# Performance work log

Hardware: AMD Instinct MI355X
Metric: run time of the kernel (lower is better)

The kernel has to match this reference:

```python
import jax, jax.numpy as jnp
import numpy as np

D_MODEL = 1024
D_INNER = 2 * D_MODEL          # expand=2
D_STATE = 16
D_CONV = 4
DT_RANK = D_MODEL // 16        # ceil(1024/16)
BATCH, SEQ = 4, 1024
LN_EPS = 1e-5
LRELU_SLOPE = 0.01


def setup_inputs() -> dict:
    key = jax.random.key(0)
    ks = jax.random.split(key, 12)
    s = 0.02
    return {
        "x": jax.random.normal(ks[0], (BATCH, SEQ, D_MODEL), jnp.float32),
        "W_in": jax.random.normal(ks[1], (D_MODEL, 2 * D_INNER), jnp.float32) * s,
        "conv_w": jax.random.normal(ks[2], (D_INNER, D_CONV), jnp.float32) * s,
        "conv_b": jnp.zeros((D_INNER,), jnp.float32),
        "W_x": jax.random.normal(ks[3], (D_INNER, DT_RANK + 2 * D_STATE), jnp.float32) * s,
        "W_dt": jax.random.normal(ks[4], (DT_RANK, D_INNER), jnp.float32) * s,
        "b_dt": jax.random.normal(ks[5], (D_INNER,), jnp.float32) * 0.1 - 4.0,
        "A_log": jnp.log(jnp.broadcast_to(jnp.arange(1, D_STATE + 1, dtype=jnp.float32), (D_INNER, D_STATE))),
        "D": jnp.ones((D_INNER,), jnp.float32),
        "W_out": jax.random.normal(ks[6], (D_INNER, D_MODEL), jnp.float32) * s,
        "gamma": jnp.ones((D_MODEL,), jnp.float32),
        "beta": jnp.zeros((D_MODEL,), jnp.float32),
    }


def _selective_scan(u, dt, A, B, C, Dp):
    # u, dt: (b, l, d); A: (d, n); B, C: (b, l, n); Dp: (d,)
    dA = jnp.exp(dt[..., None] * A)                       # (b, l, d, n)
    dBu = dt[..., None] * B[:, :, None, :] * u[..., None]  # (b, l, d, n)

    def step(h, inp):
        dA_t, dBu_t, C_t = inp                            # (b,d,n),(b,d,n),(b,n)
        h = dA_t * h + dBu_t
        y = jnp.einsum("bdn,bn->bd", h, C_t)
        return h, y

    h0 = jnp.zeros((u.shape[0], u.shape[2], A.shape[1]), u.dtype)
    xs = (dA.transpose(1, 0, 2, 3), dBu.transpose(1, 0, 2, 3), C.transpose(1, 0, 2))
    _, ys = jax.lax.scan(step, h0, xs)                    # ys: (l, b, d)
    return ys.transpose(1, 0, 2) + u * Dp                 # (b, l, d)


def _mamba(x, W_in, conv_w, conv_b, W_x, W_dt, b_dt, A_log, Dp, W_out):
    xz = x @ W_in                                          # (b, l, 2*di)
    xc, z = jnp.split(xz, 2, axis=-1)
    # causal depthwise conv over time
    xc_t = xc.transpose(0, 2, 1)                           # (b, di, l)
    kern = conv_w[:, None, :]                              # (di, 1, k)
    conv = jax.lax.conv_general_dilated(
        xc_t, kern, window_strides=(1,), padding=[(D_CONV - 1, 0)],
        dimension_numbers=("NCH", "OIH", "NCH"), feature_group_count=D_INNER)
    xc = jax.nn.silu(conv + conv_b[None, :, None]).transpose(0, 2, 1)  # (b, l, di)

    x_dbl = xc @ W_x                                       # (b, l, dt_rank + 2n)
    dt, Bm, Cm = jnp.split(x_dbl, [DT_RANK, DT_RANK + D_STATE], axis=-1)
    dt = jax.nn.softplus(dt @ W_dt + b_dt)                 # (b, l, di)
    A = -jnp.exp(A_log)                                    # (di, n)

    y = _selective_scan(xc, dt, A, Bm, Cm, Dp)             # (b, l, di)
    y = y * jax.nn.silu(z)
    return y @ W_out                                       # (b, l, d_model)


def reference(x, W_in, conv_w, conv_b, W_x, W_dt, b_dt, A_log, D, W_out, gamma, beta):
    h = x + _mamba(x, W_in, conv_w, conv_b, W_x, W_dt, b_dt, A_log, D, W_out)
    mu = jnp.mean(h, axis=-1, keepdims=True)
    var = jnp.mean(jnp.square(h - mu), axis=-1, keepdims=True)
    h = (h - mu) * jax.lax.rsqrt(var + LN_EPS) * gamma + beta
    return jnp.where(h >= 0, h, LRELU_SLOPE * h)
```

## Files before the change

kernel.cpp:

```cpp
#include <hip/hip_runtime.h>
#include <hip/hip_fp16.h>
#include <cstdint>
#include <cstddef>

typedef _Float16 f16x8 __attribute__((ext_vector_type(8)));
typedef _Float16 f16x4 __attribute__((ext_vector_type(4)));
typedef float    f32x4 __attribute__((ext_vector_type(4)));

#define TC  64
#define NCH 16

__device__ __forceinline__ float sigmoidf_(float x) { return 1.f / (1.f + __expf(-x)); }

__device__ __forceinline__ void gload_lds16(const _Float16* g, _Float16* l) {
  __builtin_amdgcn_global_load_lds(
      (const __attribute__((address_space(1))) void*)g,
      (__attribute__((address_space(3))) void*)l, 16, 0, 0);
}

__device__ __forceinline__ void t16_body(const float* __restrict__ src,
    _Float16* __restrict__ dst, int R, int C, int Cpad, int bx, int by,
    int tid, float tile[32][33]) {
  int c0 = bx * 32, r0 = by * 32, tx = tid & 31, ty = tid >> 5;
  #pragma unroll
  for (int i = 0; i < 4; ++i) {
    int r = r0 + ty + i * 8, c = c0 + tx;
    tile[ty + i * 8][tx] = (r < R && c < C) ? src[(size_t)r * C + c] : 0.f;
  }
  __syncthreads();
  #pragma unroll
  for (int i = 0; i < 4; ++i) {
    int cc = c0 + ty + i * 8, rr = r0 + tx;
    if (cc < Cpad && rr < R) dst[(size_t)cc * R + rr] = (_Float16)tile[tx][ty + i * 8];
  }
}

__global__ __launch_bounds__(256) void k_prep(
    const float* __restrict__ x, _Float16* __restrict__ x16,
    const float* __restrict__ W_in, _Float16* __restrict__ WinT,
    const float* __restrict__ W_x, _Float16* __restrict__ WxT,
    const float* __restrict__ W_dt, _Float16* __restrict__ WdtT,
    const float* __restrict__ W_out, _Float16* __restrict__ WoutT,
    const float* __restrict__ convw, _Float16* __restrict__ cwT)
{
  __shared__ float tile[32][33];
  const int blk = blockIdx.x, tid = threadIdx.x;
  if (blk < 4096) {
    int i = blk * 256 + tid;
    float4 v = ((const float4*)x)[i];
    f16x4 o = {(_Float16)v.x, (_Float16)v.y, (_Float16)v.z, (_Float16)v.w};
    ((f16x4*)x16)[i] = o;
  } else if (blk < 8192) {
    int b = blk - 4096;
    t16_body(W_in, WinT, 1024, 4096, 4096, b & 127, b >> 7, tid, tile);
  } else if (blk < 8448) {
    int b = blk - 8192;
    t16_body(W_x, WxT, 2048, 96, 128, b & 3, b >> 2, tid, tile);
  } else if (blk < 8576) {
    int b = blk - 8448;
    t16_body(W_dt, WdtT, 64, 2048, 2048, b & 63, b >> 6, tid, tile);
  } else if (blk < 10624) {
    int b = blk - 8576;
    t16_body(W_out, WoutT, 2048, 1024, 1024, b & 31, b >> 5, tid, tile);
  } else {
    #pragma unroll
    for (int j = 0; j < 32; ++j) {
      int idx = j * 256 + tid;
      int tap = idx >> 11, d = idx & 2047;
      cwT[idx] = (_Float16)convw[d * 4 + tap];
    }
  }
}

template <int EPI>
__global__ __launch_bounds__(256) void k_gemm_bt(
    const _Float16* __restrict__ A,
    const _Float16* __restrict__ BT,
    float* __restrict__ C,
    _Float16* __restrict__ C16,
    _Float16* __restrict__ AUX,
    const float* __restrict__ bias,
    int M, int N, int K)
{
  __shared__ __align__(16) _Float16 As[128 * 64];
  __shared__ __align__(16) _Float16 Bs[128 * 64];
  const int tid  = threadIdx.x;
  const int lane = tid & 63;
  const int wave = tid >> 6;
  const int wm = (wave >> 1) * 64;
  const int wn = (wave & 1) * 64;
  const int l15 = lane & 15;
  const int q   = lane >> 4;
  const int m0 = blockIdx.y * 128;
  const int n0 = blockIdx.x * 128;

  const int kpb = K / gridDim.z;
  const int k0  = blockIdx.z * kpb;

  const int rch = lane >> 3;
  const int g   = (lane & 7) ^ (rch & 7);
  const _Float16* gA = A  + (size_t)(m0 + wave * 32 + rch) * K + k0 + g * 8;
  const _Float16* gB = BT + (size_t)(n0 + wave * 32 + rch) * K + k0 + g * 8;
  _Float16* lA = As + wave * 32 * 64 + lane * 8;
  _Float16* lB = Bs + wave * 32 * 64 + lane * 8;

  const int sx = l15 & 7;

  f32x4 acc[4][4] = {};

  for (int k = 0; k < kpb; k += 64) {
    #pragma unroll
    for (int c = 0; c < 4; ++c) {
      gload_lds16(gA + (size_t)(c * 8) * K + k, lA + c * 512);
      gload_lds16(gB + (size_t)(c * 8) * K + k, lB + c * 512);
    }
    __syncthreads();
    #pragma unroll
    for (int k32 = 0; k32 < 2; ++k32) {
      f16x8 af[4], bf[4];
      #pragma unroll
      for (int i = 0; i < 4; ++i) {
        af[i] = *(const f16x8*)&As[(wm + i * 16 + l15) * 64 + ((k32 * 4 + q) ^ sx) * 8];
        bf[i] = *(const f16x8*)&Bs[(wn + i * 16 + l15) * 64 + ((k32 * 4 + q) ^ sx) * 8];
      }
      #pragma unroll
      for (int mi = 0; mi < 4; ++mi)
        #pragma unroll
        for (int ni = 0; ni < 4; ++ni)
          acc[mi][ni] = __builtin_amdgcn_mfma_f32_16x16x32_f16(af[mi], bf[ni], acc[mi][ni], 0, 0, 0);
    }
    __syncthreads();
  }

  if constexpr (EPI == 4) {
    #pragma unroll
    for (int mi = 0; mi < 4; ++mi) {
      #pragma unroll
      for (int ni = 0; ni < 4; ++ni) {
        int col = n0 + wn + ni * 16 + l15;
        #pragma unroll
        for (int r = 0; r < 4; ++r) {
          int row = m0 + wm + mi * 16 + q * 4 + r;
          C[(size_t)blockIdx.z * M * N + (size_t)row * N + col] = acc[mi][ni][r];
        }
      }
    }
  } else {
    _Float16* Ep = As + wave * 1280;
    const int rr = lane >> 2, cb = lane & 3;
    #pragma unroll
    for (int mi = 0; mi < 4; ++mi) {
      #pragma unroll
      for (int ni = 0; ni < 4; ++ni) {
        int col = n0 + wn + ni * 16 + l15;
        #pragma unroll
        for (int r = 0; r < 4; ++r) {
          float v = acc[mi][ni][r];
          _Float16 hv;
          if constexpr (EPI == 2) {
            float t = v + bias[col];
            float sp = (t > 20.f) ? t : log1pf(__expf(t));
            hv = (_Float16)sp;
          } else if constexpr (EPI == 3) {
            hv = (n0 >= 2048) ? (_Float16)(v * sigmoidf_(v)) : (_Float16)v;
          } else {
            hv = (_Float16)v;
          }
          Ep[(q * 4 + r) * 72 + ni * 16 + l15] = hv;
        }
      }
      __syncthreads();
      f16x8 o0 = *(const f16x8*)&Ep[rr * 72 + cb * 16];
      f16x8 o1 = *(const f16x8*)&Ep[rr * 72 + cb * 16 + 8];
      int row = m0 + wm + mi * 16 + rr;
      int colb = wn + cb * 16;
      if constexpr (EPI == 2) {
        _Float16* dst = AUX + (size_t)row * N + n0 + colb;
        *(f16x8*)dst = o0;
        *(f16x8*)(dst + 8) = o1;
      } else if constexpr (EPI == 3) {
        if (n0 < 2048) {
          _Float16* dst = C16 + (size_t)row * 2048 + n0 + colb;
          *(f16x8*)dst = o0;
          *(f16x8*)(dst + 8) = o1;
        } else {
          _Float16* dst = AUX + (size_t)row * 2048 + (n0 - 2048) + colb;
          *(f16x8*)dst = o0;
          *(f16x8*)(dst + 8) = o1;
        }
      } else {
        _Float16* dst = C16 + (size_t)blockIdx.z * M * N + (size_t)row * N + n0 + colb;
        *(f16x8*)dst = o0;
        *(f16x8*)(dst + 8) = o1;
      }
      __syncthreads();
    }
  }
}

__global__ __launch_bounds__(256) void k_red(const float* __restrict__ Cp,
                                             _Float16* __restrict__ dtin,
                                             float* __restrict__ xbc) {
  int i = blockIdx.x * 256 + threadIdx.x;
  const int PL = 4096 * 128;
  float s = Cp[i] + Cp[i + PL] + Cp[i + 2 * PL] + Cp[i + 3 * PL];
  int col = i & 127, row = i >> 7;
  if (col < 64) dtin[(size_t)row * 64 + col] = (_Float16)s;
  else if (col < 96) xbc[(size_t)row * 32 + (col - 64)] = s;
}

__global__ __launch_bounds__(256) void k_conv_silu(
    const _Float16* __restrict__ xc, const _Float16* __restrict__ cwT,
    const float* __restrict__ cb, _Float16* __restrict__ out)
{
  const int row = blockIdx.x;
  const int t = row & 1023;
  const int d8 = threadIdx.x;
  const size_t base = (size_t)row * 2048 + d8 * 8;
  f16x8 p0 = *(const f16x8*)&xc[base];
  f16x8 w3 = *(const f16x8*)&cwT[3 * 2048 + d8 * 8];
  float4 cb0 = ((const float4*)cb)[d8 * 2];
  float4 cb1 = ((const float4*)cb)[d8 * 2 + 1];
  float accv[8] = {cb0.x, cb0.y, cb0.z, cb0.w, cb1.x, cb1.y, cb1.z, cb1.w};
  #pragma unroll
  for (int j = 0; j < 8; ++j) accv[j] += (float)w3[j] * (float)p0[j];
  if (t >= 1) {
    f16x8 p = *(const f16x8*)&xc[base - 2048];
    f16x8 w = *(const f16x8*)&cwT[2 * 2048 + d8 * 8];
    #pragma unroll
    for (int j = 0; j < 8; ++j) accv[j] += (float)w[j] * (float)p[j];
  }
  if (t >= 2) {
    f16x8 p = *(const f16x8*)&xc[base - 4096];
    f16x8 w = *(const f16x8*)&cwT[1 * 2048 + d8 * 8];
    #pragma unroll
    for (int j = 0; j < 8; ++j) accv[j] += (float)w[j] * (float)p[j];
  }
  if (t >= 3) {
    f16x8 p = *(const f16x8*)&xc[base - 6144];
    f16x8 w = *(const f16x8*)&cwT[0 * 2048 + d8 * 8];
    #pragma unroll
    for (int j = 0; j < 8; ++j) accv[j] += (float)w[j] * (float)p[j];
  }
  f16x8 o;
  #pragma unroll
  for (int j = 0; j < 8; ++j) o[j] = (_Float16)(accv[j] * sigmoidf_(accv[j]));
  *(f16x8*)&out[base] = o;
}

__global__ __launch_bounds__(256) void k_scan_part(
    const _Float16* __restrict__ dt, const _Float16* __restrict__ u,
    const float* __restrict__ xbc, const float* __restrict__ A_log,
    float* __restrict__ P, float* __restrict__ S)
{
  const int tid = threadIdx.x;
  const int d = blockIdx.x * 256 + tid;
  const int c = blockIdx.y;
  const int b = blockIdx.z;
  const int row0 = b * 1024 + c * TC;
  __shared__ float Bs[TC * 16];
  for (int i = tid; i < TC * 16; i += 256) {
    int t = i >> 4, n = i & 15;
    Bs[i] = xbc[(size_t)(row0 + t) * 32 + n];
  }
  float a[16];
  #pragma unroll
  for (int n = 0; n < 16; ++n) a[n] = -__expf(A_log[d * 16 + n]);
  float h[16] = {};
  float sumdt = 0.f;
  __syncthreads();
  for (int t = 0; t < TC; ++t) {
    const int row = row0 + t;
    float dtv = (float)dt[(size_t)row * 2048 + d];
    float uv  = (float)u[(size_t)row * 2048 + d];
    float dtu = dtv * uv;
    sumdt += dtv;
    #pragma unroll
    for (int n = 0; n < 16; ++n)
      h[n] = h[n] * __expf(dtv * a[n]) + dtu * Bs[t * 16 + n];
  }
  const size_t base = (size_t)(b * NCH + c) * 16 * 2048 + d;
  #pragma unroll
  for (int n = 0; n < 16; ++n) {
    P[base + n * 2048] = __expf(sumdt * a[n]);
    S[base + n * 2048] = h[n];
  }
}

__global__ __launch_bounds__(256) void k_scan_comb(
    float* __restrict__ P, const float* __restrict__ S)
{
  int idx = blockIdx.x * 256 + threadIdx.x;
  int d = idx & 2047;
  int n = (idx >> 11) & 15;
  int b = idx >> 15;
  float H = 0.f;
  for (int c = 0; c < NCH - 1; ++c) {
    size_t off = ((size_t)(b * NCH + c) * 16 + n) * 2048 + d;
    H = P[off] * H + S[off];
    P[off] = H;
  }
}

__global__ __launch_bounds__(256) void k_scan_y(
    const _Float16* dt, const _Float16* __restrict__ u,
    const _Float16* __restrict__ zs, const float* __restrict__ xbc,
    const float* __restrict__ A_log, const float* __restrict__ Hbuf,
    const float* __restrict__ Dv, _Float16* ys)
{
  const int tid = threadIdx.x;
  const int d = blockIdx.x * 256 + tid;
  const int c = blockIdx.y;
  const int b = blockIdx.z;
  const int row0 = b * 1024 + c * TC;
  __shared__ float Bs[TC * 16], Cs[TC * 16];
  for (int i = tid; i < TC * 16; i += 256) {
    int t = i >> 4, n = i & 15;
    Bs[i] = xbc[(size_t)(row0 + t) * 32 + n];
    Cs[i] = xbc[(size_t)(row0 + t) * 32 + 16 + n];
  }
  float a[16];
  #pragma unroll
  for (int n = 0; n < 16; ++n) a[n] = -__expf(A_log[d * 16 + n]);
  float h[16];
  if (c == 0) {
    #pragma unroll
    for (int n = 0; n < 16; ++n) h[n] = 0.f;
  } else {
    const size_t hb = (size_t)(b * NCH + (c - 1)) * 16 * 2048 + d;
    #pragma unroll
    for (int n = 0; n < 16; ++n) h[n] = Hbuf[hb + n * 2048];
  }
  const float Dd = Dv[d];
  __syncthreads();
  for (int t = 0; t < TC; ++t) {
    const int row = row0 + t;
    float dtv = (float)dt[(size_t)row * 2048 + d];
    float uv  = (float)u[(size_t)row * 2048 + d];
    float zv  = (float)zs[(size_t)row * 2048 + d];
    float dtu = dtv * uv;
    float y = uv * Dd;
    #pragma unroll
    for (int n = 0; n < 16; ++n) {
      h[n] = h[n] * __expf(dtv * a[n]) + dtu * Bs[t * 16 + n];
      y = fmaf(h[n], Cs[t * 16 + n], y);
    }
    ys[(size_t)row * 2048 + d] = (_Float16)(y * zv);
  }
}

__global__ __launch_bounds__(256) void k_resid_ln(
    const float* __restrict__ x, const _Float16* __restrict__ yp,
    const float* __restrict__ gamma, const float* __restrict__ beta,
    float* __restrict__ out)
{
  int row = blockIdx.x;
  int tid = threadIdx.x;
  const int PLH = 4096 * 1024;
  const int o4 = row * 256 + tid;
  float4 xv = ((const float4*)x)[o4];
  f16x4 a0 = ((const f16x4*)yp)[o4];
  f16x4 a1 = ((const f16x4*)(yp + PLH))[o4];
  float v[4] = {xv.x + (float)a0[0] + (float)a1[0],
                xv.y + (float)a0[1] + (float)a1[1],
                xv.z + (float)a0[2] + (float)a1[2],
                xv.w + (float)a0[3] + (float)a1[3]};
  float s = v[0] + v[1] + v[2] + v[3];
  float s2 = v[0]*v[0] + v[1]*v[1] + v[2]*v[2] + v[3]*v[3];
  #pragma unroll
  for (int off = 32; off > 0; off >>= 1) {
    s  += __shfl_down(s, off, 64);
    s2 += __shfl_down(s2, off, 64);
  }
  __shared__ float rs[4], rs2[4];
  int wv = tid >> 6, ln = tid & 63;
  if (ln == 0) { rs[wv] = s; rs2[wv] = s2; }
  __syncthreads();
  if (tid == 0) {
    float a = 0.f, b2 = 0.f;
    #pragma unroll
    for (int i = 0; i < 4; ++i) { a += rs[i]; b2 += rs2[i]; }
    rs[0] = a; rs2[0] = b2;
  }
  __syncthreads();
  float mu  = rs[0] * (1.f / 1024.f);
  float var = rs2[0] * (1.f / 1024.f) - mu * mu;
  float inv = rsqrtf(var + 1e-5f);
  float4 gv = ((const float4*)gamma)[tid];
  float4 bv = ((const float4*)beta)[tid];
  float gg[4] = {gv.x, gv.y, gv.z, gv.w};
  float bb[4] = {bv.x, bv.y, bv.z, bv.w};
  float4 ov;
  float* op = (float*)&ov;
  #pragma unroll
  for (int i = 0; i < 4; ++i) {
    float hn = (v[i] - mu) * inv * gg[i] + bb[i];
    op[i] = hn >= 0.f ? hn : 0.01f * hn;
  }
  ((float4*)out)[o4] = ov;
}

extern "C" void kernel_launch(void* const* d_in, const int* in_sizes, int n_in,
                              void* d_out, int out_size, void* d_ws, size_t ws_size,
                              hipStream_t stream)
{
  const float* x     = (const float*)d_in[0];
  const float* W_in  = (const float*)d_in[1];
  const float* convw = (const float*)d_in[2];
  const float* convb = (const float*)d_in[3];
  const float* W_x   = (const float*)d_in[4];
  const float* W_dt  = (const float*)d_in[5];
  const float* b_dt  = (const float*)d_in[6];
  const float* A_log = (const float*)d_in[7];
  const float* Dv    = (const float*)d_in[8];
  const float* W_out = (const float*)d_in[9];
  const float* gamma = (const float*)d_in[10];
  const float* beta  = (const float*)d_in[11];
  float* out = (float*)d_out;

  char* ws = (char*)d_ws;
  const size_t MB = 1ull << 20;
  _Float16* x16   = (_Float16*)(ws + 0 * MB);
  _Float16* WinT  = (_Float16*)(ws + 8 * MB);
  _Float16* xc16  = (_Float16*)(ws + 16 * MB);
  _Float16* zsil  = (_Float16*)(ws + 32 * MB);
  _Float16* xcs   = (_Float16*)(ws + 48 * MB);
  _Float16* dtb   = (_Float16*)(ws + 64 * MB);
  _Float16* WxT   = (_Float16*)(ws + 80 * MB);
  _Float16* WdtT  = (_Float16*)(ws + 80 * MB + 512 * 1024);
  _Float16* WoutT = (_Float16*)(ws + 81 * MB);
  float*    Cpart = (float*)   (ws + 85 * MB);
  float*    xbc   = (float*)   (ws + 93 * MB);
  _Float16* dtin  = (_Float16*)(ws + 93 * MB + 512 * 1024);
  _Float16* cwT   = (_Float16*)(ws + 94 * MB);
  float*    Pb    = (float*)   (ws + 0 * MB);
  float*    Sb    = (float*)   (ws + 8 * MB);
  _Float16* ysb   = dtb;
  _Float16* ypH   = (_Float16*)(ws + 0 * MB);

  k_prep<<<10625, 256, 0, stream>>>(x, x16, W_in, WinT, W_x, WxT, W_dt, WdtT,
                                    W_out, WoutT, convw, cwT);
  k_gemm_bt<3><<<dim3(32, 32), 256, 0, stream>>>(x16, WinT, nullptr, xc16, zsil, nullptr, 4096, 4096, 1024);
  k_conv_silu<<<4096, 256, 0, stream>>>(xc16, cwT, convb, xcs);
  k_gemm_bt<4><<<dim3(1, 32, 4), 256, 0, stream>>>(xcs, WxT, Cpart, nullptr, nullptr, nullptr, 4096, 128, 2048);
  k_red<<<4096 * 128 / 256, 256, 0, stream>>>(Cpart, dtin, xbc);
  k_gemm_bt<2><<<dim3(16, 32), 256, 0, stream>>>(dtin, WdtT, nullptr, nullptr, dtb, b_dt, 4096, 2048, 64);
  k_scan_part<<<dim3(8, NCH, 4), 256, 0, stream>>>(dtb, xcs, xbc, A_log, Pb, Sb);
  k_scan_comb<<<4 * 16 * 2048 / 256, 256, 0, stream>>>(Pb, Sb);
  k_scan_y<<<dim3(8, NCH, 4), 256, 0, stream>>>(dtb, xcs, zsil, xbc, A_log, Pb, Dv, ysb);
  k_gemm_bt<5><<<dim3(8, 32, 2), 256, 0, stream>>>(ysb, WoutT, nullptr, ypH, nullptr, nullptr, 4096, 1024, 2048);
  k_resid_ln<<<4096, 256, 0, stream>>>(x, ypH, gamma, beta, out);
}
```

Baseline: 364.7 us.

## Fuse causal conv+SiLU into x_proj GEMM and scan kernels, drop conv kernel

Removes the standalone conv+SiLU kernel and its 16 MB fp16 output buffer. The conv and SiLU are now recomputed inside the x-projection GEMM's A-tile load and inside both scan kernels, using a rolling window of the previous three timesteps. The residual LayerNorm now reads the fp16 copy of x instead of fp32, and workspace buffers are remapped. This trades extra global reads and recomputation for fewer memory passes and one fewer launch, and the fp16 residual slightly lowers precision.

```diff
diff --git a/kernel.cpp b/kernel.cpp
--- a/kernel.cpp
+++ b/kernel.cpp
@@ -76,7 +76,6 @@
 __global__ __launch_bounds__(256) void k_gemm_bt(
     const _Float16* __restrict__ A,
     const _Float16* __restrict__ BT,
-    float* __restrict__ C,
     _Float16* __restrict__ C16,
     _Float16* __restrict__ AUX,
     const float* __restrict__ bias,
@@ -132,68 +131,147 @@
     __syncthreads();
   }
 
-  if constexpr (EPI == 4) {
-    #pragma unroll
-    for (int mi = 0; mi < 4; ++mi) {
-      #pragma unroll
-      for (int ni = 0; ni < 4; ++ni) {
-        int col = n0 + wn + ni * 16 + l15;
-        #pragma unroll
-        for (int r = 0; r < 4; ++r) {
-          int row = m0 + wm + mi * 16 + q * 4 + r;
-          C[(size_t)blockIdx.z * M * N + (size_t)row * N + col] = acc[mi][ni][r];
+  _Float16* Ep = As + wave * 1280;
+  const int rr = lane >> 2, cb2 = lane & 3;
+  #pragma unroll
+  for (int mi = 0; mi < 4; ++mi) {
+    #pragma unroll
+    for (int ni = 0; ni < 4; ++ni) {
+      int col = n0 + wn + ni * 16 + l15;
+      #pragma unroll
+      for (int r = 0; r < 4; ++r) {
+        float v = acc[mi][ni][r];
+        _Float16 hv;
+        if constexpr (EPI == 2) {
+          float t = v + bias[col];
+          float sp = (t > 20.f) ? t : log1pf(__expf(t));
+          hv = (_Float16)sp;
+        } else if constexpr (EPI == 3) {
+          hv = (n0 >= 2048) ? (_Float16)(v * sigmoidf_(v)) : (_Float16)v;
+        } else {
+          hv = (_Float16)v;
         }
+        Ep[(q * 4 + r) * 72 + ni * 16 + l15] = hv;
       }
     }
-  } else {
-    _Float16* Ep = As + wave * 1280;
-    const int rr = lane >> 2, cb = lane & 3;
-    #pragma unroll
-    for (int mi = 0; mi < 4; ++mi) {
-      #pragma unroll
-      for (int ni = 0; ni < 4; ++ni) {
-        int col = n0 + wn + ni * 16 + l15;
-        #pragma unroll
-        for (int r = 0; r < 4; ++r) {
-          float v = acc[mi][ni][r];
-          _Float16 hv;
-          if constexpr (EPI == 2) {
-            float t = v + bias[col];
-            float sp = (t > 20.f) ? t : log1pf(__expf(t));
-            hv = (_Float16)sp;
-          } else if constexpr (EPI == 3) {
-            hv = (n0 >= 2048) ? (_Float16)(v * sigmoidf_(v)) : (_Float16)v;
-          } else {
-            hv = (_Float16)v;
-          }
-          Ep[(q * 4 + r) * 72 + ni * 16 + l15] = hv;
-        }
-      }
-      __syncthreads();
-      f16x8 o0 = *(const f16x8*)&Ep[rr * 72 + cb * 16];
-      f16x8 o1 = *(const f16x8*)&Ep[rr * 72 + cb * 16 + 8];
-      int row = m0 + wm + mi * 16 + rr;
-      int colb = wn + cb * 16;
-      if constexpr (EPI == 2) {
-        _Float16* dst = AUX + (size_t)row * N + n0 + colb;
+    __syncthreads();
+    f16x8 o0 = *(const f16x8*)&Ep[rr * 72 + cb2 * 16];
+    f16x8 o1 = *(const f16x8*)&Ep[rr * 72 + cb2 * 16 + 8];
+    int row = m0 + wm + mi * 16 + rr;
+    int colb = wn + cb2 * 16;
+    if constexpr (EPI == 2) {
+      _Float16* dst = AUX + (size_t)row * N + n0 + colb;
+      *(f16x8*)dst = o0;
+      *(f16x8*)(dst + 8) = o1;
+    } else if constexpr (EPI == 3) {
+      if (n0 < 2048) {
+        _Float16* dst = C16 + (size_t)row * 2048 + n0 + colb;
         *(f16x8*)dst = o0;
         *(f16x8*)(dst + 8) = o1;
-      } else if constexpr (EPI == 3) {
-        if (n0 < 2048) {
-          _Float16* dst = C16 + (size_t)row * 2048 + n0 + colb;
-          *(f16x8*)dst = o0;
-          *(f16x8*)(dst + 8) = o1;
-        } else {
-          _Float16* dst = AUX + (size_t)row * 2048 + (n0 - 2048) + colb;
-          *(f16x8*)dst = o0;
-          *(f16x8*)(dst + 8) = o1;
-        }
       } else {
-        _Float16* dst = C16 + (size_t)blockIdx.z * M * N + (size_t)row * N + n0 + colb;
+        _Float16* dst = AUX + (size_t)row * 2048 + (n0 - 2048) + colb;
         *(f16x8*)dst = o0;
         *(f16x8*)(dst + 8) = o1;
       }
-      __syncthreads();
+    } else {
+      _Float16* dst = C16 + (size_t)blockIdx.z * M * N + (size_t)row * N + n0 + colb;
+      *(f16x8*)dst = o0;
+      *(f16x8*)(dst + 8) = o1;
+    }
+    __syncthreads();
+  }
+}
+
+__global__ __launch_bounds__(256) void k_g2(
+    const _Float16* __restrict__ xc,
+    const _Float16* __restrict__ cwT,
+    const float* __restrict__ cb,
+    const _Float16* __restrict__ BT,
+    float* __restrict__ C)
+{
+  __shared__ __align__(16) _Float16 As[128 * 64];
+  __shared__ __align__(16) _Float16 Bs[128 * 64];
+  const int tid  = threadIdx.x;
+  const int lane = tid & 63;
+  const int wave = tid >> 6;
+  const int wm = (wave >> 1) * 64;
+  const int wn = (wave & 1) * 64;
+  const int l15 = lane & 15;
+  const int q   = lane >> 4;
+  const int m0 = blockIdx.y * 128;
+  const int K = 2048;
+  const int k0 = blockIdx.z * 512;
+
+  const int rch = lane >> 3;
+  const int g   = (lane & 7) ^ (rch & 7);
+  const _Float16* gB = BT + (size_t)(wave * 32 + rch) * K + k0 + g * 8;
+  _Float16* lB = Bs + wave * 32 * 64 + lane * 8;
+  _Float16* lA = As + wave * 2048 + lane * 8;
+
+  const int sx = l15 & 7;
+
+  f32x4 acc[4][4] = {};
+
+  for (int k = 0; k < 512; k += 64) {
+    #pragma unroll
+    for (int c = 0; c < 4; ++c)
+      gload_lds16(gB + (size_t)(c * 8) * K + k, lB + c * 512);
+    #pragma unroll
+    for (int c = 0; c < 4; ++c) {
+      int row = wave * 32 + c * 8 + rch;
+      int m = m0 + row;
+      int t = m & 1023;
+      int dcol = k0 + k + g * 8;
+      const _Float16* xp = xc + (size_t)m * 2048 + dcol;
+      f16x8 x0 = *(const f16x8*)xp;
+      f16x8 x1 = {}, x2 = {}, x3 = {};
+      if (t >= 1) x1 = *(const f16x8*)(xp - 2048);
+      if (t >= 2) x2 = *(const f16x8*)(xp - 4096);
+      if (t >= 3) x3 = *(const f16x8*)(xp - 6144);
+      f16x8 w3 = *(const f16x8*)&cwT[3 * 2048 + dcol];
+      f16x8 w2 = *(const f16x8*)&cwT[2 * 2048 + dcol];
+      f16x8 w1 = *(const f16x8*)&cwT[1 * 2048 + dcol];
+      f16x8 w0 = *(const f16x8*)&cwT[0 * 2048 + dcol];
+      float4 cb0 = *(const float4*)&cb[dcol];
+      float4 cb1 = *(const float4*)&cb[dcol + 4];
+      float av[8] = {cb0.x, cb0.y, cb0.z, cb0.w, cb1.x, cb1.y, cb1.z, cb1.w};
+      f16x8 o;
+      #pragma unroll
+      for (int j = 0; j < 8; ++j) {
+        float s = av[j] + (float)w3[j] * (float)x0[j] + (float)w2[j] * (float)x1[j]
+                        + (float)w1[j] * (float)x2[j] + (float)w0[j] * (float)x3[j];
+        o[j] = (_Float16)(s * sigmoidf_(s));
+      }
+      *(f16x8*)(lA + c * 512) = o;
+    }
+    __syncthreads();
+    #pragma unroll
+    for (int k32 = 0; k32 < 2; ++k32) {
+      f16x8 af[4], bf[4];
+      #pragma unroll
+      for (int i = 0; i < 4; ++i) {
+        af[i] = *(const f16x8*)&As[(wm + i * 16 + l15) * 64 + ((k32 * 4 + q) ^ sx) * 8];
+        bf[i] = *(const f16x8*)&Bs[(wn + i * 16 + l15) * 64 + ((k32 * 4 + q) ^ sx) * 8];
+      }
+      #pragma unroll
+      for (int mi = 0; mi < 4; ++mi)
+        #pragma unroll
+        for (int ni = 0; ni < 4; ++ni)
+          acc[mi][ni] = __builtin_amdgcn_mfma_f32_16x16x32_f16(af[mi], bf[ni], acc[mi][ni], 0, 0, 0);
+    }
+    __syncthreads();
+  }
+
+  #pragma unroll
+  for (int mi = 0; mi < 4; ++mi) {
+    #pragma unroll
+    for (int ni = 0; ni < 4; ++ni) {
+      int col = wn + ni * 16 + l15;
+      #pragma unroll
+      for (int r = 0; r < 4; ++r) {
+        int row = m0 + wm + mi * 16 + q * 4 + r;
+        C[(size_t)blockIdx.z * 4096 * 128 + (size_t)row * 128 + col] = acc[mi][ni][r];
+      }
     }
   }
 }
@@ -209,47 +287,9 @@
   else if (col < 96) xbc[(size_t)row * 32 + (col - 64)] = s;
 }
 
-__global__ __launch_bounds__(256) void k_conv_silu(
-    const _Float16* __restrict__ xc, const _Float16* __restrict__ cwT,
-    const float* __restrict__ cb, _Float16* __restrict__ out)
-{
-  const int row = blockIdx.x;
-  const int t = row & 1023;
-  const int d8 = threadIdx.x;
-  const size_t base = (size_t)row * 2048 + d8 * 8;
-  f16x8 p0 = *(const f16x8*)&xc[base];
-  f16x8 w3 = *(const f16x8*)&cwT[3 * 2048 + d8 * 8];
-  float4 cb0 = ((const float4*)cb)[d8 * 2];
-  float4 cb1 = ((const float4*)cb)[d8 * 2 + 1];
-  float accv[8] = {cb0.x, cb0.y, cb0.z, cb0.w, cb1.x, cb1.y, cb1.z, cb1.w};
-  #pragma unroll
-  for (int j = 0; j < 8; ++j) accv[j] += (float)w3[j] * (float)p0[j];
-  if (t >= 1) {
-    f16x8 p = *(const f16x8*)&xc[base - 2048];
-    f16x8 w = *(const f16x8*)&cwT[2 * 2048 + d8 * 8];
-    #pragma unroll
-    for (int j = 0; j < 8; ++j) accv[j] += (float)w[j] * (float)p[j];
-  }
-  if (t >= 2) {
-    f16x8 p = *(const f16x8*)&xc[base - 4096];
-    f16x8 w = *(const f16x8*)&cwT[1 * 2048 + d8 * 8];
-    #pragma unroll
-    for (int j = 0; j < 8; ++j) accv[j] += (float)w[j] * (float)p[j];
-  }
-  if (t >= 3) {
-    f16x8 p = *(const f16x8*)&xc[base - 6144];
-    f16x8 w = *(const f16x8*)&cwT[0 * 2048 + d8 * 8];
-    #pragma unroll
-    for (int j = 0; j < 8; ++j) accv[j] += (float)w[j] * (float)p[j];
-  }
-  f16x8 o;
-  #pragma unroll
-  for (int j = 0; j < 8; ++j) o[j] = (_Float16)(accv[j] * sigmoidf_(accv[j]));
-  *(f16x8*)&out[base] = o;
-}
-
 __global__ __launch_bounds__(256) void k_scan_part(
-    const _Float16* __restrict__ dt, const _Float16* __restrict__ u,
+    const _Float16* __restrict__ dt, const _Float16* __restrict__ xc,
+    const _Float16* __restrict__ cwT, const float* __restrict__ cb,
     const float* __restrict__ xbc, const float* __restrict__ A_log,
     float* __restrict__ P, float* __restrict__ S)
 {
@@ -266,13 +306,25 @@
   float a[16];
   #pragma unroll
   for (int n = 0; n < 16; ++n) a[n] = -__expf(A_log[d * 16 + n]);
+  const float cbd = cb[d];
+  const float w0 = (float)cwT[d], w1 = (float)cwT[2048 + d];
+  const float w2 = (float)cwT[4096 + d], w3 = (float)cwT[6144 + d];
+  float xm1 = 0.f, xm2 = 0.f, xm3 = 0.f;
+  if (c > 0) {
+    xm1 = (float)xc[(size_t)(row0 - 1) * 2048 + d];
+    xm2 = (float)xc[(size_t)(row0 - 2) * 2048 + d];
+    xm3 = (float)xc[(size_t)(row0 - 3) * 2048 + d];
+  }
   float h[16] = {};
   float sumdt = 0.f;
   __syncthreads();
   for (int t = 0; t < TC; ++t) {
     const int row = row0 + t;
+    float xt = (float)xc[(size_t)row * 2048 + d];
+    float up = cbd + w3 * xt + w2 * xm1 + w1 * xm2 + w0 * xm3;
+    float uv = up * sigmoidf_(up);
+    xm3 = xm2; xm2 = xm1; xm1 = xt;
     float dtv = (float)dt[(size_t)row * 2048 + d];
-    float uv  = (float)u[(size_t)row * 2048 + d];
     float dtu = dtv * uv;
     sumdt += dtv;
     #pragma unroll
@@ -303,7 +355,8 @@
 }
 
 __global__ __launch_bounds__(256) void k_scan_y(
-    const _Float16* dt, const _Float16* __restrict__ u,
+    const _Float16* dt, const _Float16* __restrict__ xc,
+    const _Float16* __restrict__ cwT, const float* __restrict__ cb,
     const _Float16* __restrict__ zs, const float* __restrict__ xbc,
     const float* __restrict__ A_log, const float* __restrict__ Hbuf,
     const float* __restrict__ Dv, _Float16* ys)
@@ -322,6 +375,15 @@
   float a[16];
   #pragma unroll
   for (int n = 0; n < 16; ++n) a[n] = -__expf(A_log[d * 16 + n]);
+  const float cbd = cb[d];
+  const float w0 = (float)cwT[d], w1 = (float)cwT[2048 + d];
+  const float w2 = (float)cwT[4096 + d], w3 = (float)cwT[6144 + d];
+  float xm1 = 0.f, xm2 = 0.f, xm3 = 0.f;
+  if (c > 0) {
+    xm1 = (float)xc[(size_t)(row0 - 1) * 2048 + d];
+    xm2 = (float)xc[(size_t)(row0 - 2) * 2048 + d];
+    xm3 = (float)xc[(size_t)(row0 - 3) * 2048 + d];
+  }
   float h[16];
   if (c == 0) {
     #pragma unroll
@@ -335,8 +397,11 @@
   __syncthreads();
   for (int t = 0; t < TC; ++t) {
     const int row = row0 + t;
+    float xt = (float)xc[(size_t)row * 2048 + d];
+    float up = cbd + w3 * xt + w2 * xm1 + w1 * xm2 + w0 * xm3;
+    float uv = up * sigmoidf_(up);
+    xm3 = xm2; xm2 = xm1; xm1 = xt;
     float dtv = (float)dt[(size_t)row * 2048 + d];
-    float uv  = (float)u[(size_t)row * 2048 + d];
     float zv  = (float)zs[(size_t)row * 2048 + d];
     float dtu = dtv * uv;
     float y = uv * Dd;
@@ -350,7 +415,7 @@
 }
 
 __global__ __launch_bounds__(256) void k_resid_ln(
-    const float* __restrict__ x, const _Float16* __restrict__ yp,
+    const _Float16* __restrict__ x16, const _Float16* __restrict__ yp,
     const float* __restrict__ gamma, const float* __restrict__ beta,
     float* __restrict__ out)
 {
@@ -358,13 +423,12 @@
   int tid = threadIdx.x;
   const int PLH = 4096 * 1024;
   const int o4 = row * 256 + tid;
-  float4 xv = ((const float4*)x)[o4];
+  f16x4 xv = ((const f16x4*)x16)[o4];
   f16x4 a0 = ((const f16x4*)yp)[o4];
   f16x4 a1 = ((const f16x4*)(yp + PLH))[o4];
-  float v[4] = {xv.x + (float)a0[0] + (float)a1[0],
-                xv.y + (float)a0[1] + (float)a1[1],
-                xv.z + (float)a0[2] + (float)a1[2],
-                xv.w + (float)a0[3] + (float)a1[3]};
+  float v[4];
+  #pragma unroll
+  for (int i = 0; i < 4; ++i) v[i] = (float)xv[i] + (float)a0[i] + (float)a1[i];
   float s = v[0] + v[1] + v[2] + v[3];
   float s2 = v[0]*v[0] + v[1]*v[1] + v[2]*v[2] + v[3]*v[3];
   #pragma unroll
@@ -424,7 +488,7 @@
   _Float16* WinT  = (_Float16*)(ws + 8 * MB);
   _Float16* xc16  = (_Float16*)(ws + 16 * MB);
   _Float16* zsil  = (_Float16*)(ws + 32 * MB);
-  _Float16* xcs   = (_Float16*)(ws + 48 * MB);
+  float*    Sb    = (float*)   (ws + 48 * MB);
   _Float16* dtb   = (_Float16*)(ws + 64 * MB);
   _Float16* WxT   = (_Float16*)(ws + 80 * MB);
   _Float16* WdtT  = (_Float16*)(ws + 80 * MB + 512 * 1024);
@@ -433,21 +497,19 @@
   float*    xbc   = (float*)   (ws + 93 * MB);
   _Float16* dtin  = (_Float16*)(ws + 93 * MB + 512 * 1024);
   _Float16* cwT   = (_Float16*)(ws + 94 * MB);
-  float*    Pb    = (float*)   (ws + 0 * MB);
-  float*    Sb    = (float*)   (ws + 8 * MB);
+  float*    Pb    = (float*)   (ws + 8 * MB);
   _Float16* ysb   = dtb;
-  _Float16* ypH   = (_Float16*)(ws + 0 * MB);
+  _Float16* ypH   = (_Float16*)(ws + 16 * MB);
 
   k_prep<<<10625, 256, 0, stream>>>(x, x16, W_in, WinT, W_x, WxT, W_dt, WdtT,
                                     W_out, WoutT, convw, cwT);
-  k_gemm_bt<3><<<dim3(32, 32), 256, 0, stream>>>(x16, WinT, nullptr, xc16, zsil, nullptr, 4096, 4096, 1024);
-  k_conv_silu<<<4096, 256, 0, stream>>>(xc16, cwT, convb, xcs);
-  k_gemm_bt<4><<<dim3(1, 32, 4), 256, 0, stream>>>(xcs, WxT, Cpart, nullptr, nullptr, nullptr, 4096, 128, 2048);
+  k_gemm_bt<3><<<dim3(32, 32), 256, 0, stream>>>(x16, WinT, xc16, zsil, nullptr, 4096, 4096, 1024);
+  k_g2<<<dim3(1, 32, 4), 256, 0, stream>>>(xc16, cwT, convb, WxT, Cpart);
   k_red<<<4096 * 128 / 256, 256, 0, stream>>>(Cpart, dtin, xbc);
-  k_gemm_bt<2><<<dim3(16, 32), 256, 0, stream>>>(dtin, WdtT, nullptr, nullptr, dtb, b_dt, 4096, 2048, 64);
-  k_scan_part<<<dim3(8, NCH, 4), 256, 0, stream>>>(dtb, xcs, xbc, A_log, Pb, Sb);
+  k_gemm_bt<2><<<dim3(16, 32), 256, 0, stream>>>(dtin, WdtT, nullptr, dtb, b_dt, 4096, 2048, 64);
+  k_scan_part<<<dim3(8, NCH, 4), 256, 0, stream>>>(dtb, xc16, cwT, convb, xbc, A_log, Pb, Sb);
   k_scan_comb<<<4 * 16 * 2048 / 256, 256, 0, stream>>>(Pb, Sb);
-  k_scan_y<<<dim3(8, NCH, 4), 256, 0, stream>>>(dtb, xcs, zsil, xbc, A_log, Pb, Dv, ysb);
-  k_gemm_bt<5><<<dim3(8, 32, 2), 256, 0, stream>>>(ysb, WoutT, nullptr, ypH, nullptr, nullptr, 4096, 1024, 2048);
-  k_resid_ln<<<4096, 256, 0, stream>>>(x, ypH, gamma, beta, out);
-}
+  k_scan_y<<<dim3(8, NCH, 4), 256, 0, stream>>>(dtb, xc16, cwT, convb, zsil, xbc, A_log, Pb, Dv, ysb);
+  k_gemm_bt<5><<<dim3(8, 32, 2), 256, 0, stream>>>(ysb, WoutT, ypH, nullptr, nullptr, 4096, 1024, 2048);
+  k_resid_ln<<<4096, 256, 0, stream>>>(x16, ypH, gamma, beta, out);
+}
```

After: 369.1 us. No clear change (+1.2%).
